# Performance work log

Measured on AMD Instinct MI355X. Metric: run time of the kernel, lower is better.

## Reference

```python
import jax, jax.numpy as jnp
import numpy as np

DIM, HEADS = 1024, 16
HD = DIM // HEADS  # head_dim = 64
EPS = 1e-5


def setup_inputs() -> dict:
    key = jax.random.key(0)
    ks = jax.random.split(key, 8)
    B, N = 2, 2048
    x = jax.random.normal(ks[0], (B, N, DIM), dtype=jnp.float32)
    # RoPE table: [N, HD//2, 2] = (cos, sin) per position/freq
    inv_freq = 1.0 / (10000.0 ** (jnp.arange(0, HD, 2, dtype=jnp.float32) / HD))  # [HD//2]
    angles = jnp.arange(N, dtype=jnp.float32)[:, None] * inv_freq[None, :]        # [N, HD//2]
    freq_cis = jnp.stack([jnp.cos(angles), jnp.sin(angles)], axis=-1)             # [N, HD//2, 2]
    s = 0.02
    Wqkv = jax.random.normal(ks[1], (DIM, 3 * DIM), dtype=jnp.float32) * s
    ln_q_g = jnp.ones((HD,), jnp.float32)
    ln_q_b = jnp.zeros((HD,), jnp.float32)
    ln_k_g = jnp.ones((HD,), jnp.float32)
    ln_k_b = jnp.zeros((HD,), jnp.float32)
    Wproj = jax.random.normal(ks[2], (DIM, DIM), dtype=jnp.float32) * s
    bproj = jnp.zeros((DIM,), jnp.float32)
    return {"x": x, "freq_cis": freq_cis, "Wqkv": Wqkv,
            "ln_q_g": ln_q_g, "ln_q_b": ln_q_b, "ln_k_g": ln_k_g, "ln_k_b": ln_k_b,
            "Wproj": Wproj, "bproj": bproj}


def _layernorm(t, g, b):
    mu = jnp.mean(t, axis=-1, keepdims=True)
    var = jnp.mean(jnp.square(t - mu), axis=-1, keepdims=True)
    return (t - mu) * jax.lax.rsqrt(var + EPS) * g + b


def _rope(t, cos, sin):
    # t: [b, n, h, hd]; pairs are interleaved (even=real, odd=imag)
    b, n, h, hd = t.shape
    tr = jnp.transpose(t[..., 0::2], (0, 2, 1, 3))  # [b, h, n, hd//2]
    ti = jnp.transpose(t[..., 1::2], (0, 2, 1, 3))
    out_r = tr * cos - ti * sin
    out_i = tr * sin + ti * cos
    return jnp.stack([out_r, out_i], axis=-1).reshape(b, h, n, hd)  # [b, h, n, hd]


def reference(x, freq_cis, Wqkv, ln_q_g, ln_q_b, ln_k_g, ln_k_b, Wproj, bproj):
    B, N, _ = x.shape
    qkv = (x @ Wqkv).reshape(B, N, 3, HEADS, HD)  # split is outermost in the packed dim
    q, k, v = qkv[:, :, 0], qkv[:, :, 1], qkv[:, :, 2]  # [b, n, h, hd]
    q = _layernorm(q, ln_q_g, ln_q_b)
    k = _layernorm(k, ln_k_g, ln_k_b)
    cos = freq_cis[None, None, :, :, 0]  # [1, 1, n, hd//2]
    sin = freq_cis[None, None, :, :, 1]
    q = _rope(q, cos, sin)  # [b, h, n, hd]
    k = _rope(k, cos, sin)
    v = jnp.transpose(v, (0, 2, 1, 3))  # [b, h, n, hd]
    scores = jnp.einsum('bhqd,bhkd->bhqk', q, k) * (1.0 / np.sqrt(HD))
    attn = jax.nn.softmax(scores, axis=-1)
    out = jnp.einsum('bhqk,bhkd->bhqd', attn, v)
    out = jnp.transpose(out, (0, 2, 1, 3)).reshape(B, N, HEADS * HD)
    return out @ Wproj + bproj
```

## Files before the change

kernel.cpp:

```cpp
#include <hip/hip_runtime.h>

typedef __bf16 bf16_t;
typedef bf16_t bf16x8 __attribute__((ext_vector_type(8)));
typedef bf16_t bf16x4 __attribute__((ext_vector_type(4)));
typedef float f32x4 __attribute__((ext_vector_type(4)));
typedef short s16x4 __attribute__((ext_vector_type(4)));

typedef __attribute__((address_space(1))) void* as1_void;
typedef __attribute__((address_space(3))) void* as3_void;

static constexpr int kDim   = 1024;
static constexpr int kHeads = 16;
static constexpr int kHd    = 64;
static constexpr int kBatch = 2;
static constexpr int kSeq   = 2048;
static constexpr int kM     = kBatch * kSeq;
static constexpr int kNqkv  = 3 * kDim;
static constexpr float kQScale = 0.125f * 1.4426950408889634f;
static constexpr float kFixedMax = 16.0f;

__device__ __forceinline__ void gld_lds16(const bf16_t* g, bf16_t* l) {
  __builtin_amdgcn_global_load_lds((as1_void)(void*)const_cast<bf16_t*>(g),
                                   (as3_void)(void*)l, 16, 0, 0);
}

__device__ __forceinline__ f32x4 mfma16(s16x4 a, s16x4 b, f32x4 c) {
#if __has_builtin(__builtin_amdgcn_mfma_f32_16x16x16bf16_1k)
  return __builtin_amdgcn_mfma_f32_16x16x16bf16_1k(a, b, c, 0, 0, 0);
#else
  f32x4 d;
  asm volatile("v_mfma_f32_16x16x16_bf16 %0, %1, %2, %3"
               : "=v"(d) : "v"(a), "v"(b), "v"(c));
  return d;
#endif
}

__device__ __forceinline__ unsigned pack2_bf16(float lo, float hi) {
  unsigned a = __builtin_bit_cast(unsigned, lo) + 0x8000u;
  unsigned b = __builtin_bit_cast(unsigned, hi) + 0x8000u;
  return __builtin_amdgcn_perm(b, a, 0x07060302u);
}

__global__ __launch_bounds__(256) void prep(const float* __restrict__ x, bf16_t* __restrict__ xb,
                                            const float* __restrict__ Wqkv, bf16_t* __restrict__ WqkvT,
                                            const float* __restrict__ Wproj, bf16_t* __restrict__ WprojT) {
  __shared__ float tile[32][33];
  const int bid = blockIdx.x, tid = threadIdx.x;
  if (bid < 1024) {
#pragma unroll
    for (int j = 0; j < 4; ++j) {
      const int i = bid * 1024 + j * 256 + tid;
      const float4 f = ((const float4*)x)[i];
      bf16x4 o;
      o[0] = (bf16_t)f.x; o[1] = (bf16_t)f.y; o[2] = (bf16_t)f.z; o[3] = (bf16_t)f.w;
      ((bf16x4*)xb)[i] = o;
    }
    return;
  }
  const float* in; bf16_t* out; int R, C, t;
  if (bid < 4096) { in = Wqkv;  out = WqkvT;  R = kDim; C = kNqkv; t = bid - 1024; }
  else            { in = Wproj; out = WprojT; R = kDim; C = kDim;  t = bid - 4096; }
  const int ntx = C / 32;
  const int c0 = (t % ntx) * 32, r0 = (t / ntx) * 32;
  const int tx = tid & 31, ty = tid >> 5;
#pragma unroll
  for (int j = 0; j < 4; ++j)
    tile[ty + 8 * j][tx] = in[(size_t)(r0 + ty + 8 * j) * C + (c0 + tx)];
  __syncthreads();
#pragma unroll
  for (int j = 0; j < 4; ++j)
    out[(size_t)(c0 + ty + 8 * j) * R + (r0 + tx)] = (bf16_t)tile[tx][ty + 8 * j];
}

__global__ __launch_bounds__(256) void gemm_proj_64(const bf16_t* __restrict__ A,
                                                    const bf16_t* __restrict__ Bt,
                                                    float* __restrict__ Cout,
                                                    const float* __restrict__ bias) {
  const int N = kDim, K = kDim;
  __shared__ __align__(16) bf16_t lA[64 * 32];
  __shared__ __align__(16) bf16_t lB[128 * 32];
  const int tid  = threadIdx.x;
  const int w    = tid >> 6, lane = tid & 63;
  const int quad = lane >> 4, l16 = lane & 15;
  const int m0 = blockIdx.y * 64, n0 = blockIdx.x * 128;

  const int strow = tid >> 2;
  const int stcol = (tid & 3) * 8;
  const bf16_t* gA = A  + (size_t)(m0 + strow) * K + stcol;
  const bf16_t* gB = Bt + (size_t)(n0 + strow) * K + stcol;
  bf16_t* lA0 = lA + w * 512;
  bf16_t* lB0 = lB + w * 512;
  bf16_t* lB1 = lB + 2048 + w * 512;

  f32x4 acc[4][2];
#pragma unroll
  for (int i = 0; i < 4; ++i)
#pragma unroll
    for (int j = 0; j < 2; ++j)
#pragma unroll
      for (int r = 0; r < 4; ++r) acc[i][j][r] = 0.f;

  for (int kb = 0; kb < (K >> 5); ++kb) {
    const int k0 = kb * 32;
    __syncthreads();
    gld_lds16(gA + k0, lA0);
    gld_lds16(gB + k0, lB0);
    gld_lds16(gB + (size_t)64 * K + k0, lB1);
    __syncthreads();
    bf16x8 af[4], bfr[2];
#pragma unroll
    for (int mt = 0; mt < 4; ++mt)
      af[mt] = *(const bf16x8*)(lA + (mt * 16 + l16) * 32 + quad * 8);
#pragma unroll
    for (int nt = 0; nt < 2; ++nt)
      bfr[nt] = *(const bf16x8*)(lB + (w * 32 + nt * 16 + l16) * 32 + quad * 8);
#pragma unroll
    for (int mt = 0; mt < 4; ++mt)
#pragma unroll
      for (int nt = 0; nt < 2; ++nt)
        acc[mt][nt] = __builtin_amdgcn_mfma_f32_16x16x32_bf16(af[mt], bfr[nt], acc[mt][nt], 0, 0, 0);
  }

#pragma unroll
  for (int mt = 0; mt < 4; ++mt)
#pragma unroll
    for (int nt = 0; nt < 2; ++nt)
#pragma unroll
      for (int r = 0; r < 4; ++r) {
        const int row = m0 + mt * 16 + quad * 4 + r;
        const int col = n0 + w * 32 + nt * 16 + l16;
        Cout[(size_t)row * N + col] = acc[mt][nt][r] + bias[col];
      }
}

__global__ __launch_bounds__(256) void gemm_qkv_fused(
    const bf16_t* __restrict__ A, const bf16_t* __restrict__ Bt,
    const float* __restrict__ freq,
    const float* __restrict__ gq, const float* __restrict__ bq,
    const float* __restrict__ gk, const float* __restrict__ bk,
    bf16_t* __restrict__ Q, bf16_t* __restrict__ Kout, bf16_t* __restrict__ Vt) {
  __shared__ __align__(16) char smem[34816];
  bf16_t* lA = (bf16_t*)smem;
  bf16_t* lB = lA + 128 * 32;
  const int tid  = threadIdx.x;
  const int w    = tid >> 6, lane = tid & 63;
  const int quad = lane >> 4, l16 = lane & 15;
  const int wm = w >> 1, wn = w & 1;
  const int m0 = blockIdx.y * 128, n0 = blockIdx.x * 128;
  const int K = kDim;

  const int strow = tid >> 2;
  const int stcol = (tid & 3) * 8;
  const bf16_t* gA = A  + (size_t)(m0 + strow) * K + stcol;
  const bf16_t* gB = Bt + (size_t)(n0 + strow) * K + stcol;
  bf16_t* lA0 = lA + w * 512;
  bf16_t* lA1 = lA + 2048 + w * 512;
  bf16_t* lB0 = lB + w * 512;
  bf16_t* lB1 = lB + 2048 + w * 512;

  f32x4 acc[4][4];
#pragma unroll
  for (int i = 0; i < 4; ++i)
#pragma unroll
    for (int j = 0; j < 4; ++j)
#pragma unroll
      for (int r = 0; r < 4; ++r) acc[i][j][r] = 0.f;

  for (int kb = 0; kb < (K >> 5); ++kb) {
    const int k0 = kb * 32;
    __syncthreads();
    gld_lds16(gA + k0, lA0);
    gld_lds16(gA + (size_t)64 * K + k0, lA1);
    gld_lds16(gB + k0, lB0);
    gld_lds16(gB + (size_t)64 * K + k0, lB1);
    __syncthreads();
    bf16x8 af[4], bfr[4];
#pragma unroll
    for (int mt = 0; mt < 4; ++mt)
      af[mt] = *(const bf16x8*)(lA + (wm * 64 + mt * 16 + l16) * 32 + quad * 8);
#pragma unroll
    for (int nt = 0; nt < 4; ++nt)
      bfr[nt] = *(const bf16x8*)(lB + (wn * 64 + nt * 16 + l16) * 32 + quad * 8);
#pragma unroll
    for (int mt = 0; mt < 4; ++mt)
#pragma unroll
      for (int nt = 0; nt < 4; ++nt)
        acc[mt][nt] = __builtin_amdgcn_mfma_f32_16x16x32_bf16(af[mt], bfr[nt], acc[mt][nt], 0, 0, 0);
  }

  const int mat = n0 >> 10;
  const int cin = (n0 & 1023) + wn * 64;
  const int h   = cin >> 6;
  const int bb  = m0 >> 11;
  const int bh  = bb * kHeads + h;
  const int nrow0 = (m0 & 2047) + wm * 64;

  if (mat == 2) {
#pragma unroll
    for (int mt = 0; mt < 4; ++mt)
#pragma unroll
      for (int nt = 0; nt < 4; ++nt) {
        bf16x4 pk;
#pragma unroll
        for (int r = 0; r < 4; ++r) pk[r] = (bf16_t)acc[mt][nt][r];
        const int d = nt * 16 + l16;
        *(bf16x4*)(Vt + ((size_t)bh * kHd + d) * kSeq + nrow0 + mt * 16 + quad * 4) = pk;
      }
    return;
  }

  __syncthreads();
  float* fsm = (float*)smem;
  {
    const int row = tid >> 1, half = tid & 1;
    const float4* src = (const float4*)(freq + ((size_t)(m0 & 2047) + row) * 64 + half * 32);
    float4* dst4 = (float4*)(fsm + row * 68 + half * 32);
#pragma unroll
    for (int j = 0; j < 8; ++j) dst4[j] = src[j];
  }
  __syncthreads();

  const float* gv_ = (mat == 0) ? gq : gk;
  const float* bv_ = (mat == 0) ? bq : bk;
  float gv[4], bv[4];
#pragma unroll
  for (int nt = 0; nt < 4; ++nt) { gv[nt] = gv_[nt * 16 + l16]; bv[nt] = bv_[nt * 16 + l16]; }
  bf16_t* dst = (mat == 0) ? Q : Kout;
  const float sgn = (l16 & 1) ? 1.f : -1.f;
  const float scl = (mat == 0) ? kQScale : 1.f;

#pragma unroll
  for (int mt = 0; mt < 4; ++mt) {
    float mu[4], inv[4];
#pragma unroll
    for (int r = 0; r < 4; ++r) {
      float s = acc[mt][0][r] + acc[mt][1][r] + acc[mt][2][r] + acc[mt][3][r];
      s += __shfl_xor(s, 1); s += __shfl_xor(s, 2);
      s += __shfl_xor(s, 4); s += __shfl_xor(s, 8);
      mu[r] = s * (1.f / 64.f);
    }
#pragma unroll
    for (int r = 0; r < 4; ++r) {
      float vs = 0.f;
#pragma unroll
      for (int nt = 0; nt < 4; ++nt) {
        const float dd = acc[mt][nt][r] - mu[r];
        vs += dd * dd;
      }
      vs += __shfl_xor(vs, 1); vs += __shfl_xor(vs, 2);
      vs += __shfl_xor(vs, 4); vs += __shfl_xor(vs, 8);
      inv[r] = rsqrtf(vs * (1.f / 64.f) + 1e-5f);
    }
#pragma unroll
    for (int nt = 0; nt < 4; ++nt) {
#pragma unroll
      for (int r = 0; r < 4; ++r) {
        const float y = (acc[mt][nt][r] - mu[r]) * inv[r] * gv[nt] + bv[nt];
        const float part = __shfl_xor(y, 1);
        const int mloc = wm * 64 + mt * 16 + quad * 4 + r;
        const float2 cs = *(const float2*)(fsm + mloc * 68 + ((nt * 16 + l16) & ~1));
        const float outv = (y * cs.x + sgn * part * cs.y) * scl;
        dst[((size_t)bh * kSeq + nrow0 + mt * 16 + quad * 4 + r) * kHd + nt * 16 + l16] =
            (bf16_t)outv;
      }
    }
  }
}

__global__ __launch_bounds__(256) void flash_attn11(const bf16_t* __restrict__ Q,
                                                    const bf16_t* __restrict__ K,
                                                    const bf16_t* __restrict__ Vt,
                                                    bf16_t* __restrict__ Op0,
                                                    bf16_t* __restrict__ Op1,
                                                    float* __restrict__ rsum) {
  __shared__ __align__(16) bf16_t lK[2][64 * 72];
  __shared__ __align__(16) bf16_t lV[2][64 * 72];
  const int tid  = threadIdx.x;
  const int w    = tid >> 6, lane = tid & 63;
  const int quad = lane >> 4, l16 = lane & 15;
  const int bh = blockIdx.x & 31;
  const int t2 = blockIdx.x >> 5;
  const int qb = t2 & 15;
  const int sp = t2 >> 4;
  const int b = bh >> 4, h = bh & 15;
  const int q0 = qb * 128 + w * 32;
  const int kv0 = sp * (kSeq / 2);
  const bf16_t* Qb = Q  + (size_t)bh * kSeq * kHd;
  const bf16_t* Kb = K  + (size_t)bh * kSeq * kHd + (size_t)kv0 * kHd;
  const bf16_t* Vb = Vt + (size_t)bh * kHd * kSeq + kv0;

  bf16x8 qf[2][2];
#pragma unroll
  for (int nt = 0; nt < 2; ++nt)
#pragma unroll
    for (int ks = 0; ks < 2; ++ks)
      qf[nt][ks] = *(const bf16x8*)(Qb + (size_t)(q0 + nt * 16 + l16) * kHd + ks * 32 + quad * 8);

  s16x4 onesA;
#pragma unroll
  for (int j = 0; j < 4; ++j) onesA[j] = (l16 == 0) ? (short)0x3F80 : (short)0;

  const int srow = tid >> 2;
  const int scol = (tid & 3) * 16;

  bf16x8 kreg[2], vreg[2];
#pragma unroll
  for (int p = 0; p < 2; ++p) {
    kreg[p] = *(const bf16x8*)(Kb + (size_t)srow * kHd + scol + 8 * p);
    vreg[p] = *(const bf16x8*)(Vb + (size_t)srow * kSeq + scol + 8 * p);
  }
#pragma unroll
  for (int p = 0; p < 2; ++p) {
    *(bf16x8*)(&lK[0][srow * 72 + scol + 8 * p]) = kreg[p];
    *(bf16x8*)(&lV[0][srow * 72 + scol + 8 * p]) = vreg[p];
  }
#pragma unroll
  for (int p = 0; p < 2; ++p) {
    kreg[p] = *(const bf16x8*)(Kb + (size_t)(64 + srow) * kHd + scol + 8 * p);
    vreg[p] = *(const bf16x8*)(Vb + (size_t)srow * kSeq + 64 + scol + 8 * p);
  }
  __syncthreads();

  f32x4 o[4][2];
  f32x4 osum[2];
#pragma unroll
  for (int nt = 0; nt < 2; ++nt) {
#pragma unroll
    for (int r = 0; r < 4; ++r) osum[nt][r] = 0.f;
#pragma unroll
    for (int ntd = 0; ntd < 4; ++ntd)
#pragma unroll
      for (int r = 0; r < 4; ++r) o[ntd][nt][r] = 0.f;
  }

  const int nIter = kSeq / 128;

  for (int it = 0; it < nIter; ++it) {
    const int cur = it & 1;
    if (it + 1 < nIter) {
#pragma unroll
      for (int p = 0; p < 2; ++p) {
        *(bf16x8*)(&lK[cur ^ 1][srow * 72 + scol + 8 * p]) = kreg[p];
        *(bf16x8*)(&lV[cur ^ 1][srow * 72 + scol + 8 * p]) = vreg[p];
      }
      if (it + 2 < nIter) {
        const int kvn = (it + 2) * 64;
#pragma unroll
        for (int p = 0; p < 2; ++p) {
          kreg[p] = *(const bf16x8*)(Kb + (size_t)(kvn + srow) * kHd + scol + 8 * p);
          vreg[p] = *(const bf16x8*)(Vb + (size_t)srow * kSeq + kvn + scol + 8 * p);
        }
      }
    }

    f32x4 st[4][2];
#pragma unroll
    for (int mt = 0; mt < 4; ++mt)
#pragma unroll
      for (int nt = 0; nt < 2; ++nt)
#pragma unroll
        for (int r = 0; r < 4; ++r) st[mt][nt][r] = -kFixedMax;
#pragma unroll
    for (int ks = 0; ks < 2; ++ks) {
      bf16x8 kf[4];
#pragma unroll
      for (int mt = 0; mt < 4; ++mt)
        kf[mt] = *(const bf16x8*)(&lK[cur][(mt * 16 + l16) * 72 + ks * 32 + quad * 8]);
#pragma unroll
      for (int mt = 0; mt < 4; ++mt)
#pragma unroll
        for (int nt = 0; nt < 2; ++nt)
          st[mt][nt] = __builtin_amdgcn_mfma_f32_16x16x32_bf16(kf[mt], qf[nt][ks], st[mt][nt], 0, 0, 0);
    }

    s16x4 pb[4][2];
#pragma unroll
    for (int mt = 0; mt < 4; ++mt)
#pragma unroll
      for (int nt = 0; nt < 2; ++nt) {
        float e0 = exp2f(st[mt][nt][0]);
        float e1 = exp2f(st[mt][nt][1]);
        float e2 = exp2f(st[mt][nt][2]);
        float e3 = exp2f(st[mt][nt][3]);
        uint2 u;
        u.x = pack2_bf16(e0, e1);
        u.y = pack2_bf16(e2, e3);
        pb[mt][nt] = __builtin_bit_cast(s16x4, u);
      }

#pragma unroll
    for (int mt = 0; mt < 4; ++mt) {
#pragma unroll
      for (int ntd = 0; ntd < 4; ++ntd) {
        const s16x4 va = *(const s16x4*)(&lV[cur][(ntd * 16 + l16) * 72 + mt * 16 + quad * 4]);
#pragma unroll
        for (int nt = 0; nt < 2; ++nt)
          o[ntd][nt] = mfma16(va, pb[mt][nt], o[ntd][nt]);
      }
#pragma unroll
      for (int nt = 0; nt < 2; ++nt)
        osum[nt] = mfma16(onesA, pb[mt][nt], osum[nt]);
    }
    __syncthreads();
  }

  if (quad == 0) {
#pragma unroll
    for (int nt = 0; nt < 2; ++nt)
      rsum[((size_t)sp * 32 + bh) * kSeq + q0 + nt * 16 + l16] = osum[nt][0];
  }

  bf16_t* op = sp ? Op1 : Op0;
#pragma unroll
  for (int nt = 0; nt < 2; ++nt) {
    const int row = q0 + nt * 16 + l16;
#pragma unroll
    for (int ntd = 0; ntd < 4; ++ntd) {
      bf16x4 ov;
#pragma unroll
      for (int r = 0; r < 4; ++r) ov[r] = (bf16_t)o[ntd][nt][r];
      *(bf16x4*)(op + ((size_t)(b * kSeq + row)) * kDim + h * kHd + ntd * 16 + quad * 4) = ov;
    }
  }
}

__global__ __launch_bounds__(256) void combine(bf16_t* __restrict__ p0,
                                               const bf16_t* __restrict__ p1,
                                               const float* __restrict__ rs) {
  const int tid = threadIdx.x;
  const int row = blockIdx.x * 2 + (tid >> 7);
  const int col = (tid & 127) * 8;
  const int h = col >> 6;
  const int b = row >> 11;
  const int r = row & 2047;
  const int bh = b * kHeads + h;
  const float inv = 1.f / (rs[(size_t)bh * kSeq + r] + rs[(size_t)(32 + bh) * kSeq + r]);
  const size_t idx = (size_t)row * kDim + col;
  const bf16x8 a = *(const bf16x8*)(p0 + idx);
  const bf16x8 c = *(const bf16x8*)(p1 + idx);
  bf16x8 o;
#pragma unroll
  for (int j = 0; j < 8; ++j) o[j] = (bf16_t)(((float)a[j] + (float)c[j]) * inv);
  *(bf16x8*)(p0 + idx) = o;
}

extern "C" void kernel_launch(void* const* d_in, const int* in_sizes, int n_in,
                              void* d_out, int out_size, void* d_ws, size_t ws_size,
                              hipStream_t stream) {
  const float* x     = (const float*)d_in[0];
  const float* freq  = (const float*)d_in[1];
  const float* Wqkv  = (const float*)d_in[2];
  const float* gq    = (const float*)d_in[3];
  const float* bq    = (const float*)d_in[4];
  const float* gk    = (const float*)d_in[5];
  const float* bk    = (const float*)d_in[6];
  const float* Wproj = (const float*)d_in[7];
  const float* bproj = (const float*)d_in[8];
  float* out = (float*)d_out;

  char* ws = (char*)d_ws;
  bf16_t* xb     = (bf16_t*)(ws + 0);
  bf16_t* WqkvT  = (bf16_t*)(ws + 8388608);
  bf16_t* WprojT = (bf16_t*)(ws + 14680064);
  bf16_t* Qb     = (bf16_t*)(ws + 16777216);
  bf16_t* Kb     = (bf16_t*)(ws + 25165824);
  bf16_t* Vtb    = (bf16_t*)(ws + 33554432);
  bf16_t* part0  = (bf16_t*)(ws + 41943040);
  bf16_t* part1  = (bf16_t*)(ws + 0);
  float*  rsum   = (float*)(ws + 8388608);

  prep<<<dim3(5120), dim3(256), 0, stream>>>(x, xb, Wqkv, WqkvT, Wproj, WprojT);
  gemm_qkv_fused<<<dim3(kNqkv / 128, kM / 128), dim3(256), 0, stream>>>(
      xb, WqkvT, freq, gq, bq, gk, bk, Qb, Kb, Vtb);
  flash_attn11<<<dim3((kSeq / 128) * 2 * kBatch * kHeads), dim3(256), 0, stream>>>(
      Qb, Kb, Vtb, part0, part1, rsum);
  combine<<<dim3(kM / 2), dim3(256), 0, stream>>>(part0, part1, rsum);
  gemm_proj_64<<<dim3(kDim / 128, kM / 64), dim3(256), 0, stream>>>(part0, WprojT, out, bproj);
}
```

Baseline: 234.5 us.

## Stage K/V tiles via direct global-to-LDS loads with XOR-swizzled layout

Replaces the register-staged K/V prefetch (global load into registers, then LDS store) with direct global_load_lds 16-byte transfers into an unpadded, XOR-swizzled LDS layout, and interleaves the QK, exp and PV steps per 16-row key tile. It also adds an occupancy hint of 4 blocks per CU to launch_bounds. The aim is to cut register pressure and VGPR round-trips, shrink the LDS footprint, and raise occupancy. The price is that the stage issued in each iteration has no explicit wait before the next barrier, so correctness depends on compiler-inserted vmcnt handling. The tighter register cap may also cause spills.

```diff
diff --git a/kernel.cpp b/kernel.cpp
--- a/kernel.cpp
+++ b/kernel.cpp
@@ -267,14 +267,14 @@
   }
 }
 
-__global__ __launch_bounds__(256) void flash_attn11(const bf16_t* __restrict__ Q,
-                                                    const bf16_t* __restrict__ K,
-                                                    const bf16_t* __restrict__ Vt,
-                                                    bf16_t* __restrict__ Op0,
-                                                    bf16_t* __restrict__ Op1,
-                                                    float* __restrict__ rsum) {
-  __shared__ __align__(16) bf16_t lK[2][64 * 72];
-  __shared__ __align__(16) bf16_t lV[2][64 * 72];
+__global__ __launch_bounds__(256, 4) void flash_attn12(const bf16_t* __restrict__ Q,
+                                                       const bf16_t* __restrict__ K,
+                                                       const bf16_t* __restrict__ Vt,
+                                                       bf16_t* __restrict__ Op0,
+                                                       bf16_t* __restrict__ Op1,
+                                                       float* __restrict__ rsum) {
+  __shared__ __align__(16) bf16_t lK[2][4096];
+  __shared__ __align__(16) bf16_t lV[2][4096];
   const int tid  = threadIdx.x;
   const int w    = tid >> 6, lane = tid & 63;
   const int quad = lane >> 4, l16 = lane & 15;
@@ -300,26 +300,25 @@
 #pragma unroll
   for (int j = 0; j < 4; ++j) onesA[j] = (l16 == 0) ? (short)0x3F80 : (short)0;
 
-  const int srow = tid >> 2;
-  const int scol = (tid & 3) * 16;
-
-  bf16x8 kreg[2], vreg[2];
-#pragma unroll
-  for (int p = 0; p < 2; ++p) {
-    kreg[p] = *(const bf16x8*)(Kb + (size_t)srow * kHd + scol + 8 * p);
-    vreg[p] = *(const bf16x8*)(Vb + (size_t)srow * kSeq + scol + 8 * p);
-  }
-#pragma unroll
-  for (int p = 0; p < 2; ++p) {
-    *(bf16x8*)(&lK[0][srow * 72 + scol + 8 * p]) = kreg[p];
-    *(bf16x8*)(&lV[0][srow * 72 + scol + 8 * p]) = vreg[p];
-  }
-#pragma unroll
-  for (int p = 0; p < 2; ++p) {
-    kreg[p] = *(const bf16x8*)(Kb + (size_t)(64 + srow) * kHd + scol + 8 * p);
-    vreg[p] = *(const bf16x8*)(Vb + (size_t)srow * kSeq + 64 + scol + 8 * p);
-  }
-  __syncthreads();
+  const int r0s = (w * 2 + 0) * 8 + (lane >> 3);
+  const int r1s = (w * 2 + 1) * 8 + (lane >> 3);
+  const int ch  = lane & 7;
+  const bf16_t* kS0 = Kb + (size_t)r0s * kHd + (ch ^ (r0s & 7)) * 8;
+  const bf16_t* kS1 = Kb + (size_t)r1s * kHd + (ch ^ (r1s & 7)) * 8;
+  const bf16_t* vS0 = Vb + (size_t)r0s * kSeq + (ch ^ (r0s & 7)) * 8;
+  const bf16_t* vS1 = Vb + (size_t)r1s * kSeq + (ch ^ (r1s & 7)) * 8;
+  bf16_t* dK0 = &lK[0][(w * 2 + 0) * 512];
+  bf16_t* dK1 = &lK[0][(w * 2 + 1) * 512];
+  bf16_t* dV0 = &lV[0][(w * 2 + 0) * 512];
+  bf16_t* dV1 = &lV[0][(w * 2 + 1) * 512];
+
+  auto stage = [&](int buf, int tile) {
+    const int lo = buf * 0;
+    gld_lds16(kS0 + (size_t)tile * 4096, dK0 + buf * 4096 + lo);
+    gld_lds16(kS1 + (size_t)tile * 4096, dK1 + buf * 4096);
+    gld_lds16(vS0 + (size_t)tile * 64,   dV0 + buf * 4096);
+    gld_lds16(vS1 + (size_t)tile * 64,   dV1 + buf * 4096);
+  };
 
   f32x4 o[4][2];
   f32x4 osum[2];
@@ -335,71 +334,45 @@
 
   const int nIter = kSeq / 128;
 
+  stage(0, 0);
+  __syncthreads();
+
   for (int it = 0; it < nIter; ++it) {
     const int cur = it & 1;
-    if (it + 1 < nIter) {
-#pragma unroll
-      for (int p = 0; p < 2; ++p) {
-        *(bf16x8*)(&lK[cur ^ 1][srow * 72 + scol + 8 * p]) = kreg[p];
-        *(bf16x8*)(&lV[cur ^ 1][srow * 72 + scol + 8 * p]) = vreg[p];
-      }
-      if (it + 2 < nIter) {
-        const int kvn = (it + 2) * 64;
-#pragma unroll
-        for (int p = 0; p < 2; ++p) {
-          kreg[p] = *(const bf16x8*)(Kb + (size_t)(kvn + srow) * kHd + scol + 8 * p);
-          vreg[p] = *(const bf16x8*)(Vb + (size_t)srow * kSeq + kvn + scol + 8 * p);
-        }
-      }
-    }
-
-    f32x4 st[4][2];
-#pragma unroll
-    for (int mt = 0; mt < 4; ++mt)
+    if (it + 1 < nIter) stage(cur ^ 1, it + 1);
+
+    const int swl = l16 & 7;
+#pragma unroll
+    for (int mt = 0; mt < 4; ++mt) {
+      bf16x8 kf0 = *(const bf16x8*)(&lK[cur][(mt * 16 + l16) * 64 + ((0 * 4 + quad) ^ swl) * 8]);
+      bf16x8 kf1 = *(const bf16x8*)(&lK[cur][(mt * 16 + l16) * 64 + ((4 + quad) ^ swl) * 8]);
+      f32x4 st[2];
+#pragma unroll
+      for (int nt = 0; nt < 2; ++nt) {
+#pragma unroll
+        for (int r = 0; r < 4; ++r) st[nt][r] = -kFixedMax;
+        st[nt] = __builtin_amdgcn_mfma_f32_16x16x32_bf16(kf0, qf[nt][0], st[nt], 0, 0, 0);
+        st[nt] = __builtin_amdgcn_mfma_f32_16x16x32_bf16(kf1, qf[nt][1], st[nt], 0, 0, 0);
+      }
+      s16x4 pb[2];
+#pragma unroll
+      for (int nt = 0; nt < 2; ++nt) {
+        uint2 u;
+        u.x = pack2_bf16(exp2f(st[nt][0]), exp2f(st[nt][1]));
+        u.y = pack2_bf16(exp2f(st[nt][2]), exp2f(st[nt][3]));
+        pb[nt] = __builtin_bit_cast(s16x4, u);
+      }
+#pragma unroll
+      for (int ntd = 0; ntd < 4; ++ntd) {
+        const s16x4 va = *(const s16x4*)(&lV[cur][(ntd * 16 + l16) * 64 +
+                                                  ((2 * mt + (quad >> 1)) ^ swl) * 8 + (quad & 1) * 4]);
+#pragma unroll
+        for (int nt = 0; nt < 2; ++nt)
+          o[ntd][nt] = mfma16(va, pb[nt], o[ntd][nt]);
+      }
 #pragma unroll
       for (int nt = 0; nt < 2; ++nt)
-#pragma unroll
-        for (int r = 0; r < 4; ++r) st[mt][nt][r] = -kFixedMax;
-#pragma unroll
-    for (int ks = 0; ks < 2; ++ks) {
-      bf16x8 kf[4];
-#pragma unroll
-      for (int mt = 0; mt < 4; ++mt)
-        kf[mt] = *(const bf16x8*)(&lK[cur][(mt * 16 + l16) * 72 + ks * 32 + quad * 8]);
-#pragma unroll
-      for (int mt = 0; mt < 4; ++mt)
-#pragma unroll
-        for (int nt = 0; nt < 2; ++nt)
-          st[mt][nt] = __builtin_amdgcn_mfma_f32_16x16x32_bf16(kf[mt], qf[nt][ks], st[mt][nt], 0, 0, 0);
-    }
-
-    s16x4 pb[4][2];
-#pragma unroll
-    for (int mt = 0; mt < 4; ++mt)
-#pragma unroll
-      for (int nt = 0; nt < 2; ++nt) {
-        float e0 = exp2f(st[mt][nt][0]);
-        float e1 = exp2f(st[mt][nt][1]);
-        float e2 = exp2f(st[mt][nt][2]);
-        float e3 = exp2f(st[mt][nt][3]);
-        uint2 u;
-        u.x = pack2_bf16(e0, e1);
-        u.y = pack2_bf16(e2, e3);
-        pb[mt][nt] = __builtin_bit_cast(s16x4, u);
-      }
-
-#pragma unroll
-    for (int mt = 0; mt < 4; ++mt) {
-#pragma unroll
-      for (int ntd = 0; ntd < 4; ++ntd) {
-        const s16x4 va = *(const s16x4*)(&lV[cur][(ntd * 16 + l16) * 72 + mt * 16 + quad * 4]);
-#pragma unroll
-        for (int nt = 0; nt < 2; ++nt)
-          o[ntd][nt] = mfma16(va, pb[mt][nt], o[ntd][nt]);
-      }
-#pragma unroll
-      for (int nt = 0; nt < 2; ++nt)
-        osum[nt] = mfma16(onesA, pb[mt][nt], osum[nt]);
+        osum[nt] = mfma16(onesA, pb[nt], osum[nt]);
     }
     __syncthreads();
   }
@@ -472,7 +445,7 @@
   prep<<<dim3(5120), dim3(256), 0, stream>>>(x, xb, Wqkv, WqkvT, Wproj, WprojT);
   gemm_qkv_fused<<<dim3(kNqkv / 128, kM / 128), dim3(256), 0, stream>>>(
       xb, WqkvT, freq, gq, bq, gk, bk, Qb, Kb, Vtb);
-  flash_attn11<<<dim3((kSeq / 128) * 2 * kBatch * kHeads), dim3(256), 0, stream>>>(
+  flash_attn12<<<dim3((kSeq / 128) * 2 * kBatch * kHeads), dim3(256), 0, stream>>>(
       Qb, Kb, Vtb, part0, part1, rsum);
   combine<<<dim3(kM / 2), dim3(256), 0, stream>>>(part0, part1, rsum);
   gemm_proj_64<<<dim3(kDim / 128, kM / 64), dim3(256), 0, stream>>>(part0, WprojT, out, bproj);
```

Result: no change. 233.2 us (-0.6%).
